# Performance work log

Hardware: AMD Instinct MI355X
Metric: run time of the kernel (lower is better)

## Reference

```python
import jax, jax.numpy as jnp
import numpy as np

B, S, E, HID, NTR, NCAL, CW, VOCAB, POS = 4096, 201, 32, 512, 4, 8, 16, 32, 256
LN_EPS = 1e-5


def _ln(x, g, b):
    m = x.mean(-1, keepdims=True)
    v = ((x - m) ** 2).mean(-1, keepdims=True)
    return (x - m) * jax.lax.rsqrt(v + LN_EPS) * g + b


def setup_inputs() -> dict:
    key = jax.random.key(0)
    ks = jax.random.split(key, 24)
    g = lambda i, shape, s=0.1: (jax.random.normal(ks[i], shape, jnp.float32) * s)
    return dict(
        encoded_seq=jax.random.randint(ks[0], (B, S), 0, VOCAB, jnp.int32),
        experiment_id=jax.random.randint(ks[1], (B,), 0, NCAL, jnp.int32),
        tok_emb=g(2, (VOCAB, E), 1.0),
        pos_emb=g(3, (POS, E), 1.0),
        ln1_g=jnp.ones((NTR, E)), ln1_b=jnp.zeros((NTR, E)),
        wq=g(4, (NTR, E, E)), wk=g(5, (NTR, E, E)), wv=g(6, (NTR, E, E)),
        bq=g(7, (NTR, E), 0.01), bk=g(8, (NTR, E), 0.01), bv=g(9, (NTR, E), 0.01),
        wo=g(10, (NTR, E, E)), bo=g(11, (NTR, E), 0.01),
        ln2_g=jnp.ones((NTR, E)), ln2_b=jnp.zeros((NTR, E)),
        w1=g(12, (NTR, E, HID)), b1=g(13, (NTR, HID), 0.01),
        w2=g(14, (NTR, HID, E)), b2=g(15, (NTR, E), 0.01),
        lnf_g=jnp.ones((E,)), lnf_b=jnp.zeros((E,)),
        wpen=g(16, (E, 1)), bpen=g(17, (1,), 0.01),
        wfan=g(18, (1, CW)), bfan=g(19, (CW,), 0.01),
        wcal=g(20, (NCAL, CW, 1)), bcal=g(21, (NCAL, 1), 0.01),
    )


def reference(encoded_seq, experiment_id, tok_emb, pos_emb,
              ln1_g, ln1_b, wq, wk, wv, bq, bk, bv, wo, bo,
              ln2_g, ln2_b, w1, b1, w2, b2,
              lnf_g, lnf_b, wpen, bpen, wfan, bfan, wcal, bcal):
    # embedding + positional add: [B,S,E]
    x = tok_emb[encoded_seq] + pos_emb[jnp.arange(S)]
    scale = 1.0 / jnp.sqrt(jnp.float32(E))  # num_heads=1 => head_dim=E
    for i in range(NTR):
        n = _ln(x, ln1_g[i], ln1_b[i])
        q = n @ wq[i] + bq[i]
        k = n @ wk[i] + bk[i]
        v = n @ wv[i] + bv[i]
        a = jax.nn.softmax(jnp.einsum('bqe,bke->bqk', q, k) * scale, axis=-1)
        att = jnp.einsum('bqk,bke->bqe', a, v) @ wo[i] + bo[i]
        x = x + att
        h = _ln(x, ln2_g[i], ln2_b[i])
        x = x + (jax.nn.silu(h @ w1[i] + b1[i]) @ w2[i] + b2[i])
    contrib = _ln(x, lnf_g, lnf_b) @ wpen + bpen        # [B,S,1]
    underlying = contrib.sum(axis=-2)                    # [B,1]
    pre = jax.nn.elu(underlying @ wfan + bfan)           # [B,CW]
    # all calibrator heads at once: [B,NCAL]
    all_corr = jnp.einsum('bc,ncj->bn', pre, wcal) + bcal[:, 0]
    mask = jax.nn.one_hot(experiment_id, NCAL, dtype=pre.dtype)  # exactly the (exp==id) mask-sum
    corrected = (all_corr * mask).sum(-1, keepdims=True) + underlying
    return corrected.squeeze()
```

## Files before the change

### kernel.cpp

```cpp
#include <hip/hip_runtime.h>


#define SS   201
#define SP   208
#define NMT  13
#define EE   32
#define HIDN 512
#define NTRL 4
#define CWN  16
#define BB   4096
#define XST  36
#define VWST 228

#define X_OFF    0
#define K_OFF    14976
#define VWT_OFF  29952
#define QS_OFF   44544
#define MS_OFF   49152
#define RS_OFF   49984
#define BIAS_OFF 50816
#define SMEM_SZ  51840

#define WS_FRAG  0
#define WS_BIAS  294912
#define WS_B1    299008
#define WS_FIN   307200
#define L2E      1.4426950408889634f

typedef unsigned short u16;
typedef unsigned int   u32;
typedef short bf16x4 __attribute__((ext_vector_type(4)));
typedef short bf16x8 __attribute__((ext_vector_type(8)));
typedef float f32x4  __attribute__((ext_vector_type(4)));
typedef float f32x2  __attribute__((ext_vector_type(2)));

__device__ __forceinline__ f32x4 MF(bf16x8 a, bf16x8 b, f32x4 c){
  return __builtin_amdgcn_mfma_f32_16x16x32_bf16(a, b, c, 0, 0, 0);
}
__device__ __forceinline__ float bf2f(u16 u){ return __uint_as_float(((u32)u)<<16); }
__device__ __forceinline__ u16 f2bf(float f){
  u32 u = __float_as_uint(f);
  u += 0x7fffu + ((u>>16)&1u);
  return (u16)(u>>16);
}
__device__ __forceinline__ u32 pk2bf(f32x2 v){
#if defined(__has_builtin) && __has_builtin(__builtin_amdgcn_cvt_pk_bf16_f32)
  auto r = __builtin_amdgcn_cvt_pk_bf16_f32(v.x, v.y);
  u32 u; __builtin_memcpy(&u, &r, 4); return u;
#else
  return ((__float_as_uint(v.x)+0x8000u)>>16) | ((__float_as_uint(v.y)+0x8000u) & 0xffff0000u);
#endif
}
__device__ __forceinline__ f32x2 upk2(u32 d){
  return f32x2{ __uint_as_float(d<<16), __uint_as_float(d & 0xffff0000u) };
}
template<bool F32>
__device__ __forceinline__ float ldv(const void* p, int i){
  if (F32) return ((const float*)p)[i];
  return bf2f(((const u16*)p)[i]);
}
template<bool F32>
__device__ __forceinline__ u16 ldbf(const void* p, int i){
  if (F32) return f2bf(((const float*)p)[i]);
  return ((const u16*)p)[i];
}
__device__ __forceinline__ bf16x8 cat44(bf16x4 lo, bf16x4 hi){
  bf16x8 r = {lo[0],lo[1],lo[2],lo[3],hi[0],hi[1],hi[2],hi[3]};
  return r;
}
__device__ __forceinline__ bf16x8 mk8(u32 a0, u32 a1, u32 a2, u32 a3){
  u32 t[4] = {a0,a1,a2,a3};
  bf16x8 r; __builtin_memcpy(&r, t, 16); return r;
}
__device__ __forceinline__ u32 silu_pk(float za, float zb){
  float ea = __builtin_amdgcn_exp2f(za * -L2E);
  float eb = __builtin_amdgcn_exp2f(zb * -L2E);
  float ra = __builtin_amdgcn_rcpf(1.f + ea);
  float rb = __builtin_amdgcn_rcpf(1.f + eb);
  return pk2bf(f32x2{za*ra, zb*rb});
}

__device__ __forceinline__ int sniff_bf16(const void* tok_emb, int tid){
  int sane = 0;
  if (tid < 64){
    u16 wd = ((const u16*)tok_emb)[tid];
    int e = (wd >> 7) & 0xFF;
    sane = (e >= 100 && e <= 140) ? 1 : 0;
  }
  return (__syncthreads_count(sane) >= 52) ? 1 : 0;
}

template<bool F32>
__device__ __forceinline__ void frag_body(const void* wq, const void* wk,
    const void* wv, const void* wo, const void* w1, const void* w2, void* ws)
{
  int t = blockIdx.x;
  int l = t / 72, k = t % 72;
  int lane = threadIdx.x, l16 = lane & 15, quad = lane >> 4;
  bf16x8 v;
  if (k < 8){
    int mat = k >> 1, half = k & 1;
    if (mat == 2){
      int col = half*16 + l16;
      #pragma unroll
      for (int j=0;j<8;j++){
        int a = quad*8 + j;
        float acc = 0.f;
        for (int e=0;e<EE;e++)
          acc += ldv<F32>(wv, l*1024 + a*32 + e) * ldv<F32>(wo, l*1024 + e*32 + col);
        v[j] = (short)f2bf(acc);
      }
    } else {
      const void* src = (mat==0)? wq : (mat==1)? wk : wo;
      #pragma unroll
      for (int j=0;j<8;j++)
        v[j] = (short)ldbf<F32>(src, l*1024 + (quad*8+j)*32 + half*16 + l16);
    }
  } else if (k < 40){
    int nt = k - 8;
    #pragma unroll
    for (int j=0;j<8;j++)
      v[j] = (short)ldbf<F32>(w1, l*16384 + (quad*8+j)*512 + nt*16 + l16);
  } else {
    int kc = (k-40)>>1, nh = (k-40)&1;
    #pragma unroll
    for (int j=0;j<8;j++){
      int hh = kc*32 + ((j&4) ? 16 : 0) + quad*4 + (j&3);
      v[j] = (short)ldbf<F32>(w2, l*16384 + hh*32 + nh*16 + l16);
    }
  }
  *(bf16x8*)((char*)ws + WS_FRAG + t*1024 + lane*16) = v;
}

__global__ __launch_bounds__(64) void fmt_frags(
    const void* __restrict__ tok_emb,
    const void* __restrict__ wq, const void* __restrict__ wk,
    const void* __restrict__ wv, const void* __restrict__ wo,
    const void* __restrict__ w1, const void* __restrict__ w2,
    void* __restrict__ ws)
{
  if (sniff_bf16(tok_emb, threadIdx.x)) frag_body<false>(wq,wk,wv,wo,w1,w2,ws);
  else                                  frag_body<true >(wq,wk,wv,wo,w1,w2,ws);
}

template<bool F32>
__device__ __forceinline__ void bias_body(
    const void* bq, const void* bk, const void* bv, const void* wo, const void* bo,
    const void* ln1_g, const void* ln1_b, const void* ln2_g, const void* ln2_b,
    const void* b1, const void* b2,
    const void* lnf_g, const void* lnf_b, const void* wpen, const void* bpen,
    const void* wfan, const void* bfan, const void* wcal, const void* bcal,
    void* ws)
{
  int tid = threadIdx.x, idx = tid & 31, grp = tid >> 5;
  float* BW  = (float*)((char*)ws + WS_BIAS);
  float* BW1 = (float*)((char*)ws + WS_B1);
  float* FW  = (float*)((char*)ws + WS_FIN);
  for (int l=0;l<NTRL;l++){
    float v = 0.f;
    switch(grp){
      case 0: v = ldv<F32>(bq, l*32+idx); break;
      case 1: v = ldv<F32>(bk, l*32+idx); break;
      case 2: {
        float acc = ldv<F32>(bo, l*32+idx);
        for (int e=0;e<EE;e++) acc += ldv<F32>(bv, l*32+e) * ldv<F32>(wo, l*1024 + e*32 + idx);
        v = acc; break;
      }
      case 3: v = ldv<F32>(ln1_g, l*32+idx); break;
      case 4: v = ldv<F32>(ln1_b, l*32+idx); break;
      case 5: v = ldv<F32>(ln2_g, l*32+idx); break;
      case 6: v = ldv<F32>(ln2_b, l*32+idx); break;
      case 7: v = ldv<F32>(b2,   l*32+idx); break;
    }
    BW[l*256 + tid] = v;
  }
  for (int i=tid; i<NTRL*HIDN; i+=256) BW1[i] = ldv<F32>(b1, i);
  if (tid < 32){
    FW[tid]    = ldv<F32>(lnf_g, tid);
    FW[32+tid] = ldv<F32>(lnf_b, tid);
    FW[64+tid] = ldv<F32>(wpen, tid);
  }
  if (tid == 0) FW[96] = ldv<F32>(bpen, 0);
  if (tid < 16){ FW[97+tid] = ldv<F32>(wfan, tid); FW[113+tid] = ldv<F32>(bfan, tid); }
  if (tid < 128) FW[129+tid] = ldv<F32>(wcal, tid);
  if (tid < 8)   FW[257+tid] = ldv<F32>(bcal, tid);
}

__global__ __launch_bounds__(256) void fmt_bias(
    const void* __restrict__ tok_emb,
    const void* __restrict__ bq, const void* __restrict__ bk,
    const void* __restrict__ bv, const void* __restrict__ wo, const void* __restrict__ bo,
    const void* __restrict__ ln1_g, const void* __restrict__ ln1_b,
    const void* __restrict__ ln2_g, const void* __restrict__ ln2_b,
    const void* __restrict__ b1, const void* __restrict__ b2,
    const void* __restrict__ lnf_g, const void* __restrict__ lnf_b,
    const void* __restrict__ wpen, const void* __restrict__ bpen,
    const void* __restrict__ wfan, const void* __restrict__ bfan,
    const void* __restrict__ wcal, const void* __restrict__ bcal,
    void* __restrict__ ws)
{
  if (sniff_bf16(tok_emb, threadIdx.x))
    bias_body<false>(bq,bk,bv,wo,bo,ln1_g,ln1_b,ln2_g,ln2_b,b1,b2,
                     lnf_g,lnf_b,wpen,bpen,wfan,bfan,wcal,bcal,ws);
  else
    bias_body<true >(bq,bk,bv,wo,bo,ln1_g,ln1_b,ln2_g,ln2_b,b1,b2,
                     lnf_g,lnf_b,wpen,bpen,wfan,bfan,wcal,bcal,ws);
}

__device__ __forceinline__ void ln_stats(const u16* Xb, float* MS, float* RS, int tid){
  if (tid < SP){
    const u32* row = (const u32*)(Xb + tid*XST);
    f32x2 v[16]; f32x2 s2 = {0.f,0.f};
    #pragma unroll
    for (int i=0;i<16;i++){ f32x2 p = upk2(row[i]); v[i] = p; s2 += p; }
    float m = (s2.x + s2.y) * (1.f/EE);
    f32x2 m2 = {m, m};
    f32x2 var2 = {0.f,0.f};
    #pragma unroll
    for (int i=0;i<16;i++){ f32x2 d = v[i]-m2; var2 += d*d; }
    MS[tid] = m;
    RS[tid] = rsqrtf((var2.x+var2.y)*(1.f/EE) + 1e-5f);
  }
}

__device__ __forceinline__ bf16x8 build_nfrag(const u16* Xb, const float* MS, const float* RS,
                                              int row, int quad, const f32x2* G2, const f32x2* B2){
  const u32* raw = (const u32*)(Xb + row*XST + quad*8);
  f32x2 m2 = { MS[row], MS[row] };
  f32x2 rs2 = { RS[row], RS[row] };
  u32 o[4];
  #pragma unroll
  for (int p=0;p<4;p++){
    f32x2 x = upk2(raw[p]);
    o[p] = pk2bf((x - m2) * rs2 * G2[p] + B2[p]);
  }
  bf16x8 r; __builtin_memcpy(&r, o, 16);
  return r;
}

template<bool F32>
__device__ __forceinline__ void tr_body(
    const int* seq, const int* expid,
    const void* tok_emb, const void* pos_emb,
    const void* ws, void* out, unsigned char* smem)
{
  u16*   Xb   = (u16*)(smem + X_OFF);
  u16*   Kb   = (u16*)(smem + K_OFF);
  u16*   VWTb = (u16*)(smem + VWT_OFF);
  float* MS   = (float*)(smem + MS_OFF);
  float* RS   = (float*)(smem + RS_OFF);
  float* BIAS = (float*)(smem + BIAS_OFF);

  const int tid  = threadIdx.x;
  const int lane = tid & 63, w = tid >> 6;
  const int l16  = lane & 15, quad = lane >> 4;
  const int b    = blockIdx.x;
  const f32x4 Z  = {0.f,0.f,0.f,0.f};

  {
    const int* srow = seq + b*SS;
    for (int i = tid; i < SP*EE; i += 256){
      int s = i >> 5, e = i & 31;
      float val = 0.f;
      if (s < SS){
        int tok = srow[s];
        val = ldv<F32>(tok_emb, tok*EE + e) + ldv<F32>(pos_emb, s*EE + e);
      }
      Xb[s*XST + e] = f2bf(val);
    }
  }
  __syncthreads();

  const float qce = 0.2550546813f;
  const f32x4 qce4 = {qce, qce, qce, qce};

  for (int l = 0; l < NTRL; ++l){
    const char* wsl = (const char*)ws + WS_FRAG + l*73728;
    bf16x8 bwq0 = *(const bf16x8*)(wsl + 0*1024 + lane*16);
    bf16x8 bwq1 = *(const bf16x8*)(wsl + 1*1024 + lane*16);
    bf16x8 bwk0 = *(const bf16x8*)(wsl + 2*1024 + lane*16);
    bf16x8 bwk1 = *(const bf16x8*)(wsl + 3*1024 + lane*16);
    bf16x8 bwv0 = *(const bf16x8*)(wsl + 4*1024 + lane*16);
    bf16x8 bwv1 = *(const bf16x8*)(wsl + 5*1024 + lane*16);
    {
      const float* BW = (const float*)((const char*)ws + WS_BIAS) + l*256;
      BIAS[tid] = BW[tid];
    }
    for (int i = tid; i < 32*16; i += 256)
      VWTb[(i>>4)*VWST + 208 + (i&15)] = 0;
    ln_stats(Xb, MS, RS, tid);
    __syncthreads();

    bf16x8 aq[4];
    {
      f32x2 G2[4], B2[4];
      #pragma unroll
      for (int p=0;p<4;p++){
        G2[p] = f32x2{BIAS[96+quad*8+2*p], BIAS[96+quad*8+2*p+1]};
        B2[p] = f32x2{BIAS[128+quad*8+2*p], BIAS[128+quad*8+2*p+1]};
      }
      f32x2 bkb2 = {BIAS[32+l16], BIAS[48+l16]};
      f32x4 bq0 = *(const f32x4*)(BIAS + quad*4);
      f32x4 bq1 = *(const f32x4*)(BIAS + 16 + quad*4);
      #pragma unroll
      for (int t=0;t<4;t++){
        int m = w + 4*t;
        if (m < NMT){
          int m16 = m*16;
          bf16x8 an = build_nfrag(Xb, MS, RS, m16+l16, quad, G2, B2);
          f32x4 ck0 = MF(an, bwk0, Z), ck1 = MF(an, bwk1, Z);
          #pragma unroll
          for (int r=0;r<4;r++){
            int row = m16 + quad*4 + r;
            u32 pk = pk2bf(f32x2{ck0[r], ck1[r]} + bkb2);
            Kb[row*XST + l16]      = (u16)pk;
            Kb[row*XST + 16 + l16] = (u16)(pk>>16);
          }
          f32x4 cw0 = MF(an, bwv0, Z), cw1 = MF(an, bwv1, Z);
          #pragma unroll
          for (int r=0;r<4;r++){
            u32 pk = pk2bf(f32x2{cw0[r], cw1[r]});
            VWTb[l16*VWST      + m16 + quad*4 + r] = (u16)pk;
            VWTb[(16+l16)*VWST + m16 + quad*4 + r] = (u16)(pk>>16);
          }
          f32x4 cq0 = MF(bwq0, an, Z), cq1 = MF(bwq1, an, Z);
          f32x4 z0 = (cq0 + bq0) * qce4;
          f32x4 z1 = (cq1 + bq1) * qce4;
          aq[t] = mk8(pk2bf(f32x2{z0[0], z0[1]}), pk2bf(f32x2{z0[2], z0[3]}),
                      pk2bf(f32x2{z1[0], z1[1]}), pk2bf(f32x2{z1[2], z1[3]}));
        }
      }
    }
    __syncthreads();

    {
      const u16* vbase0 = VWTb + l16*VWST;
      const u16* vbase1 = VWTb + (16+l16)*VWST;
      f32x4 ob0 = *(const f32x4*)(BIAS + 64 + quad*4);
      f32x4 ob1 = *(const f32x4*)(BIAS + 80 + quad*4);
      #pragma unroll
      for (int t=0;t<4;t++){
        int m = w + 4*t;
        if (m < NMT){
          int m16 = m*16;
          u32 pbw[13][2];
          float part = 0.f;
          #pragma unroll
          for (int kt=0; kt<13; kt++){
            const u16* krow = Kb + (kt*16+l16)*XST;
            bf16x8 kb8 = cat44(*(const bf16x4*)(krow + quad*4),
                               *(const bf16x4*)(krow + 16 + quad*4));
            f32x4 St = MF(kb8, aq[t], Z);
            float e0 = __builtin_amdgcn_exp2f(St[0]);
            float e1 = __builtin_amdgcn_exp2f(St[1]);
            float e2 = __builtin_amdgcn_exp2f(St[2]);
            float e3 = __builtin_amdgcn_exp2f(St[3]);
            if (kt == 12){
              int kb = quad*4;
              if (kb+0 >= 9) e0 = 0.f;
              if (kb+1 >= 9) e1 = 0.f;
              if (kb+2 >= 9) e2 = 0.f;
              if (kb+3 >= 9) e3 = 0.f;
            }
            part += (e0+e1)+(e2+e3);
            pbw[kt][0] = pk2bf(f32x2{e0,e1});
            pbw[kt][1] = pk2bf(f32x2{e2,e3});
          }
          part += __shfl_xor(part, 16);
          part += __shfl_xor(part, 32);
          float inv = __builtin_amdgcn_rcpf(part);

          f32x4 o0 = Z, o1 = Z;
          #pragma unroll
          for (int c=0;c<6;c++){
            bf16x4 a0l = *(const bf16x4*)(vbase0 + c*32 + quad*4);
            bf16x4 a0h = *(const bf16x4*)(vbase0 + c*32 + 16 + quad*4);
            bf16x4 a1l = *(const bf16x4*)(vbase1 + c*32 + quad*4);
            bf16x4 a1h = *(const bf16x4*)(vbase1 + c*32 + 16 + quad*4);
            bf16x8 B8 = mk8(pbw[2*c][0], pbw[2*c][1], pbw[2*c+1][0], pbw[2*c+1][1]);
            o0 = MF(cat44(a0l, a0h), B8, o0);
            o1 = MF(cat44(a1l, a1h), B8, o1);
          }
          {
            bf16x4 a0l = *(const bf16x4*)(vbase0 + 192 + quad*4);
            bf16x4 a0h = *(const bf16x4*)(vbase0 + 208 + quad*4);
            bf16x4 a1l = *(const bf16x4*)(vbase1 + 192 + quad*4);
            bf16x4 a1h = *(const bf16x4*)(vbase1 + 208 + quad*4);
            bf16x8 B8 = mk8(pbw[12][0], pbw[12][1], 0u, 0u);
            o0 = MF(cat44(a0l, a0h), B8, o0);
            o1 = MF(cat44(a1l, a1h), B8, o1);
          }

          u32* xr = (u32*)(Xb + (m16+l16)*XST);
          {
            u32 d0 = xr[quad*2], d1 = xr[quad*2+1];
            f32x2 r01 = f32x2{o0[0],o0[1]} * inv + (upk2(d0) + f32x2{ob0[0],ob0[1]});
            f32x2 r23 = f32x2{o0[2],o0[3]} * inv + (upk2(d1) + f32x2{ob0[2],ob0[3]});
            xr[quad*2]   = pk2bf(r01);
            xr[quad*2+1] = pk2bf(r23);
            u32 d2 = xr[8+quad*2], d3 = xr[8+quad*2+1];
            f32x2 s01 = f32x2{o1[0],o1[1]} * inv + (upk2(d2) + f32x2{ob1[0],ob1[1]});
            f32x2 s23 = f32x2{o1[2],o1[3]} * inv + (upk2(d3) + f32x2{ob1[2],ob1[3]});
            xr[8+quad*2]   = pk2bf(s01);
            xr[8+quad*2+1] = pk2bf(s23);
          }
        }
      }
    }
    __syncthreads();

    ln_stats(Xb, MS, RS, tid);
    __syncthreads();

    {
      f32x2 G2[4], B2[4];
      #pragma unroll
      for (int p=0;p<4;p++){
        G2[p] = f32x2{BIAS[160+quad*8+2*p], BIAS[160+quad*8+2*p+1]};
        B2[p] = f32x2{BIAS[192+quad*8+2*p], BIAS[192+quad*8+2*p+1]};
      }
      bf16x8 anc[4];
      #pragma unroll
      for (int t=0;t<4;t++){
        int m = w + 4*t;
        if (m < NMT) anc[t] = build_nfrag(Xb, MS, RS, m*16+l16, quad, G2, B2);
      }
      f32x4 oacc[4][2];
      #pragma unroll
      for (int t=0;t<4;t++){ oacc[t][0] = Z; oacc[t][1] = Z; }
      const char* w1f = wsl + 8*1024;
      const char* w2f = wsl + 40*1024;
      const float* BW1 = (const float*)((const char*)ws + WS_B1) + l*HIDN;

      for (int hp = 0; hp < 16; ++hp){
        bf16x8 a1lo = *(const bf16x8*)(w1f + (2*hp  )*1024 + lane*16);
        bf16x8 a1hi = *(const bf16x8*)(w1f + (2*hp+1)*1024 + lane*16);
        bf16x8 a2e0 = *(const bf16x8*)(w2f + (hp*2  )*1024 + lane*16);
        bf16x8 a2e1 = *(const bf16x8*)(w2f + (hp*2+1)*1024 + lane*16);
        f32x4 b1q0 = *(const f32x4*)(BW1 + hp*32      + quad*4);
        f32x4 b1q1 = *(const f32x4*)(BW1 + hp*32 + 16 + quad*4);
        #pragma unroll
        for (int t=0;t<4;t++){
          int m = w + 4*t;
          if (m < NMT){
            f32x4 z0 = MF(a1lo, anc[t], Z) + b1q0;
            f32x4 z1 = MF(a1hi, anc[t], Z) + b1q1;
            bf16x8 H8 = mk8(silu_pk(z0[0], z0[1]), silu_pk(z0[2], z0[3]),
                            silu_pk(z1[0], z1[1]), silu_pk(z1[2], z1[3]));
            oacc[t][0] = MF(a2e0, H8, oacc[t][0]);
            oacc[t][1] = MF(a2e1, H8, oacc[t][1]);
          }
        }
      }

      f32x4 b2q0 = *(const f32x4*)(BIAS + 224 + quad*4);
      f32x4 b2q1 = *(const f32x4*)(BIAS + 240 + quad*4);
      #pragma unroll
      for (int t=0;t<4;t++){
        int m = w + 4*t;
        if (m < NMT){
          u32* xr = (u32*)(Xb + (m*16 + l16)*XST);
          u32 d0 = xr[quad*2], d1 = xr[quad*2+1];
          f32x2 r01 = f32x2{oacc[t][0][0], oacc[t][0][1]} + (upk2(d0) + f32x2{b2q0[0], b2q0[1]});
          f32x2 r23 = f32x2{oacc[t][0][2], oacc[t][0][3]} + (upk2(d1) + f32x2{b2q0[2], b2q0[3]});
          xr[quad*2]   = pk2bf(r01);
          xr[quad*2+1] = pk2bf(r23);
          u32 d2 = xr[8+quad*2], d3 = xr[8+quad*2+1];
          f32x2 s01 = f32x2{oacc[t][1][0], oacc[t][1][1]} + (upk2(d2) + f32x2{b2q1[0], b2q1[1]});
          f32x2 s23 = f32x2{oacc[t][1][2], oacc[t][1][3]} + (upk2(d3) + f32x2{b2q1[2], b2q1[3]});
          xr[8+quad*2]   = pk2bf(s01);
          xr[8+quad*2+1] = pk2bf(s23);
        }
      }
    }
    __syncthreads();
  }

  const float* FW = (const float*)((const char*)ws + WS_FIN);
  if (tid < 32){
    BIAS[tid]    = FW[tid];
    BIAS[32+tid] = FW[32+tid];
    BIAS[64+tid] = FW[64+tid];
  }
  __syncthreads();
  float part = 0.f;
  if (tid < SS){
    const u32* row = (const u32*)(Xb + tid*XST);
    f32x2 v[16]; f32x2 s2 = {0.f,0.f};
    #pragma unroll
    for (int i=0;i<16;i++){ f32x2 p = upk2(row[i]); v[i] = p; s2 += p; }
    float m = (s2.x+s2.y) * (1.f/EE);
    f32x2 m2 = {m,m};
    f32x2 var2 = {0.f,0.f};
    #pragma unroll
    for (int i=0;i<16;i++){ f32x2 d = v[i]-m2; var2 += d*d; }
    float rs = rsqrtf((var2.x+var2.y)*(1.f/EE) + 1e-5f);
    f32x2 rs2 = {rs, rs};
    f32x2 dot2 = {0.f,0.f};
    #pragma unroll
    for (int i=0;i<16;i++){
      f32x2 g  = {BIAS[2*i], BIAS[2*i+1]};
      f32x2 bb = {BIAS[32+2*i], BIAS[33+2*i]};
      f32x2 wp = {BIAS[64+2*i], BIAS[65+2*i]};
      dot2 += ((v[i]-m2)*rs2*g + bb) * wp;
    }
    part = dot2.x + dot2.y + FW[96];
  }
  #pragma unroll
  for (int off=32; off; off>>=1) part += __shfl_xor(part, off);
  float* REDF = (float*)(smem + QS_OFF);
  __syncthreads();
  if (lane == 0) REDF[w] = part;
  __syncthreads();
  if (tid == 0){
    float u = REDF[0] + REDF[1] + REDF[2] + REDF[3];
    int ex = expid[b];
    float corr = FW[257+ex];
    #pragma unroll
    for (int c = 0; c < CWN; ++c){
      float pre = u * FW[97+c] + FW[113+c];
      pre = pre > 0.f ? pre : (__expf(pre) - 1.f);
      corr += pre * FW[129 + ex*CWN + c];
    }
    float res = corr + u;
    if (F32) ((float*)out)[b] = res;
    else     ((u16*)out)[b]  = f2bf(res);
  }
}

__global__ __launch_bounds__(256, 3) void tr_kernel(
    const int* __restrict__ seq, const int* __restrict__ expid,
    const void* __restrict__ tok_emb, const void* __restrict__ pos_emb,
    const void* __restrict__ ws, void* __restrict__ out)
{
  __shared__ __align__(16) unsigned char smem[SMEM_SZ];
  if (sniff_bf16(tok_emb, threadIdx.x))
    tr_body<false>(seq, expid, tok_emb, pos_emb, ws, out, smem);
  else
    tr_body<true >(seq, expid, tok_emb, pos_emb, ws, out, smem);
}

extern "C" void kernel_launch(void* const* d_in, const int* in_sizes, int n_in,
                              void* d_out, int out_size, void* d_ws, size_t ws_size,
                              hipStream_t stream)
{
  (void)in_sizes; (void)n_in; (void)ws_size; (void)out_size;
  const void* tok_emb = d_in[2];
  fmt_frags<<<dim3(288), dim3(64), 0, stream>>>(
      tok_emb, d_in[6], d_in[7], d_in[8], d_in[12], d_in[16], d_in[18], d_ws);
  fmt_bias<<<dim3(1), dim3(256), 0, stream>>>(
      tok_emb, d_in[9], d_in[10], d_in[11], d_in[12], d_in[13],
      d_in[4], d_in[5], d_in[14], d_in[15], d_in[17], d_in[19],
      d_in[20], d_in[21], d_in[22], d_in[23],
      d_in[24], d_in[25], d_in[26], d_in[27], d_ws);
  tr_kernel<<<dim3(BB), dim3(256), 0, stream>>>(
      (const int*)d_in[0], (const int*)d_in[1], tok_emb, d_in[3], d_ws, d_out);
}
```

Baseline: 951.8 us.

## Fold biases into MFMA accumulators, packed-math SiLU, single-pass LN stats, trim smem

Bias adds for K, Q and the FFN first layer now go in as the MFMA accumulator initial value instead of separate vector adds. SiLU and the softmax exp/sum are rewritten on f32x2 so the compiler can emit packed FP32 ops. LayerNorm stats switch to a single pass (E[x^2]-m^2), and the zero padding of the VW tail is dropped by duplicating the low half in the last tile's MFMA, which also removes the unused QS shared-memory region. The aim is fewer VALU instructions and less LDS, at some risk: the one-pass variance loses precision, and the duplicated-operand trick depends on the masked probabilities being exactly zero.

```diff
diff --git a/kernel.cpp b/kernel.cpp
--- a/kernel.cpp
+++ b/kernel.cpp
@@ -15,11 +15,10 @@
 #define X_OFF    0
 #define K_OFF    14976
 #define VWT_OFF  29952
-#define QS_OFF   44544
-#define MS_OFF   49152
-#define RS_OFF   49984
-#define BIAS_OFF 50816
-#define SMEM_SZ  51840
+#define MS_OFF   44544
+#define RS_OFF   45376
+#define BIAS_OFF 46208
+#define SMEM_SZ  47232
 
 #define WS_FRAG  0
 #define WS_BIAS  294912
@@ -72,12 +71,15 @@
   u32 t[4] = {a0,a1,a2,a3};
   bf16x8 r; __builtin_memcpy(&r, t, 16); return r;
 }
-__device__ __forceinline__ u32 silu_pk(float za, float zb){
-  float ea = __builtin_amdgcn_exp2f(za * -L2E);
-  float eb = __builtin_amdgcn_exp2f(zb * -L2E);
-  float ra = __builtin_amdgcn_rcpf(1.f + ea);
-  float rb = __builtin_amdgcn_rcpf(1.f + eb);
-  return pk2bf(f32x2{za*ra, zb*rb});
+__device__ __forceinline__ u32 spk(f32x2 z){
+  const f32x2 nl2e2 = {-L2E, -L2E};
+  const f32x2 one2  = {1.f, 1.f};
+  f32x2 a = z * nl2e2;
+  f32x2 e = { __builtin_amdgcn_exp2f(a.x), __builtin_amdgcn_exp2f(a.y) };
+  f32x2 d = one2 + e;
+  f32x2 rc = { __builtin_amdgcn_rcpf(d.x), __builtin_amdgcn_rcpf(d.y) };
+  f32x2 s = z * rc;
+  return pk2bf(s);
 }
 
 __device__ __forceinline__ int sniff_bf16(const void* tok_emb, int tid){
@@ -210,16 +212,13 @@
 __device__ __forceinline__ void ln_stats(const u16* Xb, float* MS, float* RS, int tid){
   if (tid < SP){
     const u32* row = (const u32*)(Xb + tid*XST);
-    f32x2 v[16]; f32x2 s2 = {0.f,0.f};
-    #pragma unroll
-    for (int i=0;i<16;i++){ f32x2 p = upk2(row[i]); v[i] = p; s2 += p; }
+    f32x2 s2 = {0.f,0.f}, q2 = {0.f,0.f};
+    #pragma unroll
+    for (int i=0;i<16;i++){ f32x2 p = upk2(row[i]); s2 += p; q2 += p*p; }
     float m = (s2.x + s2.y) * (1.f/EE);
-    f32x2 m2 = {m, m};
-    f32x2 var2 = {0.f,0.f};
-    #pragma unroll
-    for (int i=0;i<16;i++){ f32x2 d = v[i]-m2; var2 += d*d; }
+    float v = (q2.x + q2.y) * (1.f/EE) - m*m;
     MS[tid] = m;
-    RS[tid] = rsqrtf((var2.x+var2.y)*(1.f/EE) + 1e-5f);
+    RS[tid] = rsqrtf(v + 1e-5f);
   }
 }
 
@@ -272,7 +271,7 @@
   __syncthreads();
 
   const float qce = 0.2550546813f;
-  const f32x4 qce4 = {qce, qce, qce, qce};
+  const f32x2 qce2 = {qce, qce};
 
   for (int l = 0; l < NTRL; ++l){
     const char* wsl = (const char*)ws + WS_FRAG + l*73728;
@@ -286,8 +285,6 @@
       const float* BW = (const float*)((const char*)ws + WS_BIAS) + l*256;
       BIAS[tid] = BW[tid];
     }
-    for (int i = tid; i < 32*16; i += 256)
-      VWTb[(i>>4)*VWST + 208 + (i&15)] = 0;
     ln_stats(Xb, MS, RS, tid);
     __syncthreads();
 
@@ -299,20 +296,22 @@
         G2[p] = f32x2{BIAS[96+quad*8+2*p], BIAS[96+quad*8+2*p+1]};
         B2[p] = f32x2{BIAS[128+quad*8+2*p], BIAS[128+quad*8+2*p+1]};
       }
-      f32x2 bkb2 = {BIAS[32+l16], BIAS[48+l16]};
       f32x4 bq0 = *(const f32x4*)(BIAS + quad*4);
       f32x4 bq1 = *(const f32x4*)(BIAS + 16 + quad*4);
+      float bk0s = BIAS[32+l16], bk1s = BIAS[48+l16];
+      f32x4 kc0 = {bk0s,bk0s,bk0s,bk0s};
+      f32x4 kc1 = {bk1s,bk1s,bk1s,bk1s};
       #pragma unroll
       for (int t=0;t<4;t++){
         int m = w + 4*t;
         if (m < NMT){
           int m16 = m*16;
           bf16x8 an = build_nfrag(Xb, MS, RS, m16+l16, quad, G2, B2);
-          f32x4 ck0 = MF(an, bwk0, Z), ck1 = MF(an, bwk1, Z);
+          f32x4 ck0 = MF(an, bwk0, kc0), ck1 = MF(an, bwk1, kc1);
           #pragma unroll
           for (int r=0;r<4;r++){
             int row = m16 + quad*4 + r;
-            u32 pk = pk2bf(f32x2{ck0[r], ck1[r]} + bkb2);
+            u32 pk = pk2bf(f32x2{ck0[r], ck1[r]});
             Kb[row*XST + l16]      = (u16)pk;
             Kb[row*XST + 16 + l16] = (u16)(pk>>16);
           }
@@ -323,11 +322,9 @@
             VWTb[l16*VWST      + m16 + quad*4 + r] = (u16)pk;
             VWTb[(16+l16)*VWST + m16 + quad*4 + r] = (u16)(pk>>16);
           }
-          f32x4 cq0 = MF(bwq0, an, Z), cq1 = MF(bwq1, an, Z);
-          f32x4 z0 = (cq0 + bq0) * qce4;
-          f32x4 z1 = (cq1 + bq1) * qce4;
-          aq[t] = mk8(pk2bf(f32x2{z0[0], z0[1]}), pk2bf(f32x2{z0[2], z0[3]}),
-                      pk2bf(f32x2{z1[0], z1[1]}), pk2bf(f32x2{z1[2], z1[3]}));
+          f32x4 cq0 = MF(bwq0, an, bq0), cq1 = MF(bwq1, an, bq1);
+          aq[t] = mk8(pk2bf(f32x2{cq0[0],cq0[1]}*qce2), pk2bf(f32x2{cq0[2],cq0[3]}*qce2),
+                      pk2bf(f32x2{cq1[0],cq1[1]}*qce2), pk2bf(f32x2{cq1[2],cq1[3]}*qce2));
         }
       }
     }
@@ -344,28 +341,27 @@
         if (m < NMT){
           int m16 = m*16;
           u32 pbw[13][2];
-          float part = 0.f;
+          f32x2 pacc = {0.f, 0.f};
           #pragma unroll
           for (int kt=0; kt<13; kt++){
             const u16* krow = Kb + (kt*16+l16)*XST;
             bf16x8 kb8 = cat44(*(const bf16x4*)(krow + quad*4),
                                *(const bf16x4*)(krow + 16 + quad*4));
             f32x4 St = MF(kb8, aq[t], Z);
-            float e0 = __builtin_amdgcn_exp2f(St[0]);
-            float e1 = __builtin_amdgcn_exp2f(St[1]);
-            float e2 = __builtin_amdgcn_exp2f(St[2]);
-            float e3 = __builtin_amdgcn_exp2f(St[3]);
+            f32x2 ea = { __builtin_amdgcn_exp2f(St[0]), __builtin_amdgcn_exp2f(St[1]) };
+            f32x2 eb = { __builtin_amdgcn_exp2f(St[2]), __builtin_amdgcn_exp2f(St[3]) };
             if (kt == 12){
               int kb = quad*4;
-              if (kb+0 >= 9) e0 = 0.f;
-              if (kb+1 >= 9) e1 = 0.f;
-              if (kb+2 >= 9) e2 = 0.f;
-              if (kb+3 >= 9) e3 = 0.f;
+              if (kb+0 >= 9) ea.x = 0.f;
+              if (kb+1 >= 9) ea.y = 0.f;
+              if (kb+2 >= 9) eb.x = 0.f;
+              if (kb+3 >= 9) eb.y = 0.f;
             }
-            part += (e0+e1)+(e2+e3);
-            pbw[kt][0] = pk2bf(f32x2{e0,e1});
-            pbw[kt][1] = pk2bf(f32x2{e2,e3});
-          }
+            pacc += ea + eb;
+            pbw[kt][0] = pk2bf(ea);
+            pbw[kt][1] = pk2bf(eb);
+          }
+          float part = pacc.x + pacc.y;
           part += __shfl_xor(part, 16);
           part += __shfl_xor(part, 32);
           float inv = __builtin_amdgcn_rcpf(part);
@@ -383,12 +379,10 @@
           }
           {
             bf16x4 a0l = *(const bf16x4*)(vbase0 + 192 + quad*4);
-            bf16x4 a0h = *(const bf16x4*)(vbase0 + 208 + quad*4);
             bf16x4 a1l = *(const bf16x4*)(vbase1 + 192 + quad*4);
-            bf16x4 a1h = *(const bf16x4*)(vbase1 + 208 + quad*4);
             bf16x8 B8 = mk8(pbw[12][0], pbw[12][1], 0u, 0u);
-            o0 = MF(cat44(a0l, a0h), B8, o0);
-            o1 = MF(cat44(a1l, a1h), B8, o1);
+            o0 = MF(cat44(a0l, a0l), B8, o0);
+            o1 = MF(cat44(a1l, a1l), B8, o1);
           }
 
           u32* xr = (u32*)(Xb + (m16+l16)*XST);
@@ -443,10 +437,10 @@
         for (int t=0;t<4;t++){
           int m = w + 4*t;
           if (m < NMT){
-            f32x4 z0 = MF(a1lo, anc[t], Z) + b1q0;
-            f32x4 z1 = MF(a1hi, anc[t], Z) + b1q1;
-            bf16x8 H8 = mk8(silu_pk(z0[0], z0[1]), silu_pk(z0[2], z0[3]),
-                            silu_pk(z1[0], z1[1]), silu_pk(z1[2], z1[3]));
+            f32x4 z0 = MF(a1lo, anc[t], b1q0);
+            f32x4 z1 = MF(a1hi, anc[t], b1q1);
+            bf16x8 H8 = mk8(spk(f32x2{z0[0], z0[1]}), spk(f32x2{z0[2], z0[3]}),
+                            spk(f32x2{z1[0], z1[1]}), spk(f32x2{z1[2], z1[3]}));
             oacc[t][0] = MF(a2e0, H8, oacc[t][0]);
             oacc[t][1] = MF(a2e1, H8, oacc[t][1]);
           }
@@ -508,7 +502,7 @@
   }
   #pragma unroll
   for (int off=32; off; off>>=1) part += __shfl_xor(part, off);
-  float* REDF = (float*)(smem + QS_OFF);
+  float* REDF = (float*)(smem + MS_OFF);
   __syncthreads();
   if (lane == 0) REDF[w] = part;
   __syncthreads();
```

New measurement: 882.0 us. 1.08x faster.
